# Optimization experiments

Hardware: AMD Instinct MI355X
Metric: run time of the kernel (lower is better)

## Reference

```python
import jax, jax.numpy as jnp
import numpy as np
from jax import lax

VOCAB, D, LAYERS, PAD = 10000, 200, 3, 3
B, S = 16, 512
SCALE = 0.05  # ~ torch uniform(-1/sqrt(200), 1/sqrt(200)) scale


def setup_inputs() -> dict:
    key = jax.random.key(0)
    ks = jax.random.split(key, 8)
    x = jax.random.randint(ks[0], (B, S), 0, VOCAB)
    emb = jax.random.normal(ks[1], (VOCAB, D), jnp.float32) * SCALE
    emb = emb.at[PAD].set(0.0)  # padding_idx=3 row is zeros
    w_ih = jax.random.normal(ks[2], (LAYERS, D, D), jnp.float32) * SCALE
    w_hh = jax.random.normal(ks[3], (LAYERS, D, D), jnp.float32) * SCALE
    b_ih = jax.random.normal(ks[4], (LAYERS, D), jnp.float32) * SCALE
    b_hh = jax.random.normal(ks[5], (LAYERS, D), jnp.float32) * SCALE
    fc_w = jax.random.normal(ks[6], (VOCAB, D), jnp.float32) * SCALE
    fc_b = jax.random.normal(ks[7], (VOCAB,), jnp.float32) * SCALE
    return {"x": x, "emb": emb, "w_ih": w_ih, "w_hh": w_hh,
            "b_ih": b_ih, "b_hh": b_hh, "fc_w": fc_w, "fc_b": fc_b}


def _rnn_forward(x, emb, w_ih, w_hh, b_ih, b_hh, fc_w, fc_b):
    h = emb[x]  # (B, S, D) embedding gather
    finals = []
    for l in range(LAYERS):
        # precompute input projection for the whole sequence (efficient GEMM)
        xw = jnp.einsum('bsd,hd->bsh', h, w_ih[l]) + b_ih[l] + b_hh[l]  # (B,S,D)
        w_hh_l_T = w_hh[l].T

        def step(h_prev, x_t):
            h_new = jnp.tanh(x_t + h_prev @ w_hh_l_T)
            return h_new, h_new

        h0 = jnp.zeros((x.shape[0], D), xw.dtype)
        h_last, outs = lax.scan(step, h0, jnp.swapaxes(xw, 0, 1))  # scan over time
        h = jnp.swapaxes(outs, 0, 1)  # (B, S, D)
        finals.append(h_last)
    hidden = jnp.stack(finals)  # (LAYERS, B, D) like torch RNN hidden
    logits = h @ fc_w.T + fc_b  # (B, S, VOCAB)
    return logits, hidden


def reference(x, emb, w_ih, w_hh, b_ih, b_hh, fc_w, fc_b):
    # forward always starts from zero hidden (source ignores the hidden arg)
    return _rnn_forward(x, emb, w_ih, w_hh, b_ih, b_hh, fc_w, fc_b)
```

## Files before the change

### kernel.cpp

```cpp
#include <hip/hip_runtime.h>
#include <hip/hip_bf16.h>

#define VOCAB 10000
#define D 200
#define NLAYERS 3
#define NB 16
#define NS 512
#define M 8192
#define KA 224
#define KB 232
#define NPADA 10120
#define NTILES_N 79
#define NT_TILES 5056
#define BCHUNKS 3712

#define OFF_BUF0 0u
#define OFF_BUF1 6553600u
#define OFF_WT   13107200u
#define OFF_HBF  13587200u
#define OFF_FWB  17257216u
#define OFF_STG1 21952896u
#define OFF_FLG  28506496u
#define WS_NEED  28506624u

typedef __bf16 bf16x8 __attribute__((ext_vector_type(8)));
typedef float  f32x4  __attribute__((ext_vector_type(4)));
typedef unsigned int u32x4 __attribute__((ext_vector_type(4)));
union U64x2 { unsigned long long d[2]; bf16x8 v; };

__global__ void k_wtrans(const float* __restrict__ w_ih, float* __restrict__ wt) {
    int i = blockIdx.x * blockDim.x + threadIdx.x;
    if (i < NLAYERS * D * D) {
        int l = i / (D * D);
        int r = i - l * D * D;
        int k = r / D;
        int n = r - k * D;
        wt[i] = w_ih[l * D * D + n * D + k];
    }
}

__global__ void k_fcwbf(const float* __restrict__ fc_w, __bf16* __restrict__ fwb) {
    int i = blockIdx.x * blockDim.x + threadIdx.x;
    if (i < NPADA * KB) {
        int n = i / KB;
        int k = i - n * KB;
        float v = (n < VOCAB && k < D) ? fc_w[(size_t)n * D + k] : 0.f;
        fwb[i] = (__bf16)v;
    }
}

__global__ void k_hbf2(const float* __restrict__ h, __bf16* __restrict__ hbf) {
    int i = blockIdx.x * blockDim.x + threadIdx.x;
    if (i < M * KA) {
        int m = i / KA;
        int k = i - m * KA;
        float v = (k < D) ? h[(size_t)m * D + k] : 0.f;
        hbf[i] = (__bf16)v;
    }
}

__global__ void k_zero(u32x4* __restrict__ p, int n4) {
    int i = blockIdx.x * blockDim.x + threadIdx.x;
    if (i < n4) p[i] = u32x4{0u, 0u, 0u, 0u};
}

__global__ void k_xw_emb(const int* __restrict__ x, const float* __restrict__ emb,
                         const float* __restrict__ wt,
                         const float* __restrict__ b_ih, const float* __restrict__ b_hh,
                         float* __restrict__ xw) {
    int m0 = blockIdx.x * 32;
    int n  = threadIdx.x;
    if (n >= D) return;
    float bias = b_ih[n] + b_hh[n];
    for (int g = 0; g < 8; ++g) {
        const float* r0 = emb + (size_t)x[m0 + g * 4 + 0] * D;
        const float* r1 = emb + (size_t)x[m0 + g * 4 + 1] * D;
        const float* r2 = emb + (size_t)x[m0 + g * 4 + 2] * D;
        const float* r3 = emb + (size_t)x[m0 + g * 4 + 3] * D;
        float a0 = bias, a1 = bias, a2 = bias, a3 = bias;
        for (int k = 0; k < D; k += 4) {
            #pragma unroll
            for (int kk = 0; kk < 4; ++kk) {
                float w = wt[(k + kk) * D + n];
                a0 += r0[k + kk] * w; a1 += r1[k + kk] * w;
                a2 += r2[k + kk] * w; a3 += r3[k + kk] * w;
            }
        }
        size_t o = (size_t)(m0 + g * 4) * D + n;
        xw[o] = a0; xw[o + D] = a1; xw[o + 2 * D] = a2; xw[o + 3 * D] = a3;
    }
}

__global__ void k_xw(const float* __restrict__ hin, const float* __restrict__ wt,
                     const float* __restrict__ b_ih, const float* __restrict__ b_hh,
                     float* __restrict__ xw) {
    int m0 = blockIdx.x * 32;
    int n  = threadIdx.x;
    if (n >= D) return;
    float bias = b_ih[n] + b_hh[n];
    for (int g = 0; g < 8; ++g) {
        const float* r0 = hin + (size_t)(m0 + g * 4) * D;
        float a0 = bias, a1 = bias, a2 = bias, a3 = bias;
        for (int k = 0; k < D; k += 4) {
            #pragma unroll
            for (int kk = 0; kk < 4; ++kk) {
                float w = wt[(k + kk) * D + n];
                a0 += r0[k + kk] * w; a1 += r0[D + k + kk] * w;
                a2 += r0[2 * D + k + kk] * w; a3 += r0[3 * D + k + kk] * w;
            }
        }
        size_t o = (size_t)(m0 + g * 4) * D + n;
        xw[o] = a0; xw[o + D] = a1; xw[o + 2 * D] = a2; xw[o + 3 * D] = a3;
    }
}

__device__ inline float fast_tanh(float x) {
    x = fminf(fmaxf(x, -15.f), 15.f);
    float e = __expf(2.f * x);
    return (e - 1.f) / (e + 1.f);
}

__global__ __attribute__((amdgpu_flat_work_group_size(512, 512),
                          amdgpu_waves_per_eu(2, 2)))
void k_fused(const float* __restrict__ whh_all,
             const float* __restrict__ wih_all,
             const float* __restrict__ b_ih,
             const float* __restrict__ b_hh,
             const float* __restrict__ xw0,
             unsigned* __restrict__ cells1,
             unsigned* __restrict__ cells2,
             __bf16* __restrict__ hbf,
             float* __restrict__ hidden,
             const __bf16* __restrict__ fwb,
             const float* __restrict__ fc_b,
             float* __restrict__ out,
             unsigned* __restrict__ progress,
             unsigned* __restrict__ counter) {
    __shared__ float hp0[208], hp1[208], hin[208];
    __shared__ __bf16 Bl[BCHUNKS * 8];
    __shared__ unsigned tile_s;
    const int bid = blockIdx.x;
    const int t   = threadIdx.x;

    if (bid < 48) {
        const int l   = bid >> 4;
        const int b   = bid & 15;
        const int q   = t >> 2, dg = t & 3;
        const bool act = (q < 100);
        const int  rr  = 2 * q + (dg & 1);
        const int  rrl = act ? rr : 0;
        const bool wlane = act && (dg < 2);
        const int  dstart = dg * 52;

        f32x4 wh[2][13], wi[2][13];
        #pragma unroll
        for (int j = 0; j < 2; ++j)
            #pragma unroll
            for (int i = 0; i < 13; ++i) {
                wh[j][i] = f32x4{0.f, 0.f, 0.f, 0.f};
                wi[j][i] = f32x4{0.f, 0.f, 0.f, 0.f};
            }
        if (act) {
            #pragma unroll
            for (int j = 0; j < 2; ++j) {
                const float* wr = whh_all + (size_t)l * D * D + (size_t)(2 * q + j) * D + dstart;
                #pragma unroll
                for (int i = 0; i < 11; ++i) wh[j][i] = *(const f32x4*)(wr + 4 * i);
                if (dg < 3) {
                    wh[j][11] = *(const f32x4*)(wr + 44);
                    wh[j][12] = *(const f32x4*)(wr + 48);
                }
            }
            if (l > 0) {
                #pragma unroll
                for (int j = 0; j < 2; ++j) {
                    const float* wr = wih_all + (size_t)l * D * D + (size_t)(2 * q + j) * D + dstart;
                    #pragma unroll
                    for (int i = 0; i < 11; ++i) wi[j][i] = *(const f32x4*)(wr + 4 * i);
                    if (dg < 3) {
                        wi[j][11] = *(const f32x4*)(wr + 44);
                        wi[j][12] = *(const f32x4*)(wr + 48);
                    }
                }
            }
        }
        float bias = 0.f;
        if (l > 0 && act) bias = b_ih[l * D + rr] + b_hh[l * D + rr];

        if (t < 208) { hp0[t] = 0.f; hp1[t] = 0.f; hin[t] = 0.f; }
        __syncthreads();

        const float* xrow = xw0 + (size_t)b * NS * D;
        const unsigned* sin = (l == 1) ? cells1 + (size_t)b * NS * 200
                            : (l == 2) ? cells2 + (size_t)b * NS * 200 : nullptr;
        unsigned* sout = (l == 0) ? cells1 + (size_t)b * NS * 200
                       : (l == 1) ? cells2 + (size_t)b * NS * 200 : nullptr;

        float hn_prev = 0.f;
        float xv_next = (l == 0) ? xrow[rrl] : 0.f;
        const float* hi = hin + dstart;

        #pragma unroll 1
        for (int s = 0; s < NS; ++s) {
            float xv;
            if (l == 0) {
                xv = xv_next;
                const int sn = (s + 1 < NS) ? s + 1 : NS - 1;
                xv_next = xrow[(size_t)sn * D + rrl];
            } else {
                if (t < 200) {
                    const unsigned* p = sin + (size_t)s * 200 + t;
                    unsigned v = __hip_atomic_load(p, __ATOMIC_RELAXED,
                                                   __HIP_MEMORY_SCOPE_AGENT);
                    while (v == 0u) {
                        __builtin_amdgcn_s_sleep(1);
                        v = __hip_atomic_load(p, __ATOMIC_RELAXED,
                                              __HIP_MEMORY_SCOPE_AGENT);
                    }
                    hin[t] = __builtin_bit_cast(float, ~v);
                }
                asm volatile("s_waitcnt lgkmcnt(0)" ::: "memory");
                __builtin_amdgcn_s_barrier();
                asm volatile("" ::: "memory");
                xv = bias;
            }
            const float* hr = ((s & 1) ? hp1 : hp0) + dstart;
            float* hw = (s & 1) ? hp0 : hp1;
            f32x4 ac0{0.f,0.f,0.f,0.f}, ac1{0.f,0.f,0.f,0.f};
            #pragma unroll
            for (int i = 0; i < 13; ++i) {
                f32x4 h4 = *(const f32x4*)(hr + 4 * i);
                ac0 += h4 * wh[0][i];
                ac1 += h4 * wh[1][i];
            }
            if (l > 0) {
                #pragma unroll
                for (int i = 0; i < 13; ++i) {
                    f32x4 g4 = *(const f32x4*)(hi + 4 * i);
                    ac0 += g4 * wi[0][i];
                    ac1 += g4 * wi[1][i];
                }
            }
            float s0 = (ac0.x + ac0.y) + (ac0.z + ac0.w);
            float s1 = (ac1.x + ac1.y) + (ac1.z + ac1.w);
            s0 += __shfl_xor(s0, 1);  s0 += __shfl_xor(s0, 2);
            s1 += __shfl_xor(s1, 1);  s1 += __shfl_xor(s1, 2);
            float hn = fast_tanh(xv + ((dg & 1) ? s1 : s0));
            hn_prev = hn;
            float hpart = __shfl_xor(hn, 1);
            if (wlane) {
                hw[rr] = hn;
                if (l < 2) {
                    __hip_atomic_store(sout + (size_t)s * 200 + rr,
                                       ~__builtin_bit_cast(unsigned, hn),
                                       __ATOMIC_RELAXED, __HIP_MEMORY_SCOPE_AGENT);
                }
            }
            if (l == 2 && act && dg == 0) {
                unsigned short e0 = __builtin_bit_cast(unsigned short, (__bf16)hn);
                unsigned short e1 = __builtin_bit_cast(unsigned short, (__bf16)hpart);
                unsigned pv = (unsigned)e0 | ((unsigned)e1 << 16);
                __hip_atomic_store((unsigned*)hbf + ((size_t)b * NS + s) * 112 + q,
                                   pv, __ATOMIC_RELAXED, __HIP_MEMORY_SCOPE_AGENT);
            }
            asm volatile("s_waitcnt lgkmcnt(0)" ::: "memory");
            __builtin_amdgcn_s_barrier();
            asm volatile("" ::: "memory");
            if (l == 2 && (s & 127) == 127) {
                asm volatile("s_waitcnt vmcnt(0)" ::: "memory");
                __builtin_amdgcn_s_barrier();
                if (t == 0)
                    __hip_atomic_store(progress + b, (unsigned)((s >> 7) + 1),
                                       __ATOMIC_RELAXED, __HIP_MEMORY_SCOPE_AGENT);
            }
        }
        if (wlane) hidden[(size_t)l * NB * D + b * D + rr] = hn_prev;
    } else {
        const int lane = t & 63, wv = t >> 6;
        const int wr = wv >> 2, wc = wv & 3;
        const int lr = lane & 15, lq = lane >> 4;
        const unsigned* Au = (const unsigned*)hbf;
        for (;;) {
            if (t == 0) tile_s = atomicAdd(counter, 1u);
            __syncthreads();
            const unsigned tile = tile_s;
            if (tile >= NT_TILES) break;
            const int chunk = tile / 1264;
            const int rem   = tile - chunk * 1264;
            const int nt    = rem >> 4;
            const int b     = rem & 15;
            const int m0    = (b * 4 + chunk) * 128;
            const int n0    = nt * 128;
            {
                const u32x4* src = (const u32x4*)(fwb + (size_t)n0 * KB);
                u32x4* dst = (u32x4*)Bl;
                #pragma unroll
                for (int it = 0; it < 8; ++it) {
                    int idx = t + it * 512;
                    if (idx < BCHUNKS) dst[idx] = src[idx];
                }
            }
            if (t == 0) {
                unsigned pv = __hip_atomic_load(progress + b, __ATOMIC_RELAXED,
                                                __HIP_MEMORY_SCOPE_AGENT);
                while (pv <= (unsigned)chunk) {
                    __builtin_amdgcn_s_sleep(16);
                    pv = __hip_atomic_load(progress + b, __ATOMIC_RELAXED,
                                           __HIP_MEMORY_SCOPE_AGENT);
                }
            }
            __syncthreads();
            f32x4 acc[4][2] = {};
            #pragma unroll
            for (int ks = 0; ks < 7; ++ks) {
                bf16x8 af[4], bfr[2];
                #pragma unroll
                for (int i = 0; i < 4; ++i) {
                    size_t arow = (size_t)(m0 + wr * 64 + i * 16 + lr);
                    size_t bo = arow * 112 + (size_t)(ks * 16 + lq * 4);
                    U64x2 u;
                    u.d[0] = __hip_atomic_load((const unsigned long long*)(Au + bo),
                                               __ATOMIC_RELAXED, __HIP_MEMORY_SCOPE_AGENT);
                    u.d[1] = __hip_atomic_load((const unsigned long long*)(Au + bo) + 1,
                                               __ATOMIC_RELAXED, __HIP_MEMORY_SCOPE_AGENT);
                    af[i] = u.v;
                }
                #pragma unroll
                for (int j = 0; j < 2; ++j) {
                    int brow = wc * 32 + j * 16 + lr;
                    bfr[j] = *(const bf16x8*)(Bl + brow * KB + (ks * 4 + lq) * 8);
                }
                #pragma unroll
                for (int i = 0; i < 4; ++i)
                    #pragma unroll
                    for (int j = 0; j < 2; ++j)
                        acc[i][j] = __builtin_amdgcn_mfma_f32_16x16x32_bf16(
                                        af[i], bfr[j], acc[i][j], 0, 0, 0);
            }
            #pragma unroll
            for (int j = 0; j < 2; ++j) {
                int col = n0 + wc * 32 + j * 16 + lr;
                if (col < VOCAB) {
                    float cbias = fc_b[col];
                    #pragma unroll
                    for (int i = 0; i < 4; ++i) {
                        #pragma unroll
                        for (int r = 0; r < 4; ++r) {
                            int row = m0 + wr * 64 + i * 16 + lq * 4 + r;
                            __builtin_nontemporal_store(acc[i][j][r] + cbias,
                                &out[(size_t)row * VOCAB + col]);
                        }
                    }
                }
            }
        }
    }
}

#define STEP(HR, HW, SIDX)                                                  \
    {                                                                       \
        float xv = xv_next;                                                 \
        int snext = (SIDX) + 1 < NS ? (SIDX) + 1 : NS - 1;                  \
        xv_next = xrow[(size_t)snext * D + rrl];                            \
        f32x4 ac0{0.f,0.f,0.f,0.f}, ac1{0.f,0.f,0.f,0.f};                   \
        _Pragma("unroll")                                                   \
        for (int i = 0; i < 13; ++i) {                                      \
            f32x4 h4 = *(const f32x4*)((HR) + 4 * i);                       \
            ac0 += h4 * w4[0][i];                                           \
            ac1 += h4 * w4[1][i];                                           \
        }                                                                   \
        float s0 = (ac0.x + ac0.y) + (ac0.z + ac0.w);                       \
        float s1 = (ac1.x + ac1.y) + (ac1.z + ac1.w);                       \
        s0 += __shfl_xor(s0, 1);  s0 += __shfl_xor(s0, 2);                  \
        s1 += __shfl_xor(s1, 1);  s1 += __shfl_xor(s1, 2);                  \
        float hn = fast_tanh(xv + ((dg & 1) ? s1 : s0));                    \
        hlast = hn;                                                         \
        if (wlane) {                                                        \
            (HW)[rr] = hn;                                                  \
            xrow[(size_t)(SIDX) * D + rr] = hn;                             \
        }                                                                   \
        __syncthreads();                                                    \
    }

__global__ __attribute__((amdgpu_flat_work_group_size(512, 512),
                          amdgpu_waves_per_eu(2, 2)))
void k_scan(const float* __restrict__ whh,
            float* __restrict__ io,
            float* __restrict__ hidden) {
    __shared__ float hp0[208], hp1[208];
    int t  = threadIdx.x;
    int b  = blockIdx.x;
    int q  = t >> 2;
    int dg = t & 3;
    const bool act = (q < 100);
    const int  rr  = 2 * q + (dg & 1);
    const int  rrl = act ? rr : 0;
    const bool wlane = act && (dg < 2);
    const int  dstart = dg * 52;

    f32x4 w4[2][13];
    #pragma unroll
    for (int j = 0; j < 2; ++j)
        #pragma unroll
        for (int i = 0; i < 13; ++i) w4[j][i] = f32x4{0.f, 0.f, 0.f, 0.f};
    if (act) {
        #pragma unroll
        for (int j = 0; j < 2; ++j) {
            const float* wr = whh + (size_t)(2 * q + j) * D + dstart;
            #pragma unroll
            for (int i = 0; i < 11; ++i) w4[j][i] = *(const f32x4*)(wr + 4 * i);
            if (dg < 3) {
                w4[j][11] = *(const f32x4*)(wr + 44);
                w4[j][12] = *(const f32x4*)(wr + 48);
            }
        }
    }
    if (t < 208) { hp0[t] = 0.f; hp1[t] = 0.f; }
    __syncthreads();

    float* xrow = io + (size_t)b * NS * D;
    const float* hr0 = hp0 + dstart;
    const float* hr1 = hp1 + dstart;
    float xv_next = xrow[rrl];
    float hlast = 0.f;

    #pragma unroll 1
    for (int s2 = 0; s2 < NS / 2; ++s2) {
        STEP(hr0, hp1, 2 * s2)
        STEP(hr1, hp0, 2 * s2 + 1)
    }
    if (wlane) hidden[b * D + rr] = hlast;
}

__global__ __launch_bounds__(256) void k_fc(const __bf16* __restrict__ A,
                                            const __bf16* __restrict__ Bw,
                                            const float* __restrict__ fc_b,
                                            float* __restrict__ Cout) {
    __shared__ __bf16 Bl2[3840 * 8];
    int tid = threadIdx.x;
    int wg  = blockIdx.x;
    int mt  = wg / NTILES_N, nt = wg - mt * NTILES_N;
    int m0  = mt * 128, n0 = nt * 128;
    {
        const u32x4* src = (const u32x4*)(Bw + (size_t)n0 * KB);
        u32x4* dst = (u32x4*)Bl2;
        u32x4 stg[15];
        #pragma unroll
        for (int it = 0; it < 15; ++it) stg[it] = src[tid + it * 256];
        #pragma unroll
        for (int it = 0; it < 15; ++it) dst[tid + it * 256] = stg[it];
    }
    __syncthreads();
    int lane = tid & 63, wv = tid >> 6;
    int wr = wv >> 1, wc = wv & 1;
    int lr = lane & 15, lq = lane >> 4;
    f32x4 acc[4][4] = {};
    #pragma unroll
    for (int ks = 0; ks < 7; ++ks) {
        bf16x8 af[4], bfr[4];
        #pragma unroll
        for (int i = 0; i < 4; ++i) {
            int arow = m0 + wr * 64 + i * 16 + lr;
            af[i] = *(const bf16x8*)(A + (size_t)arow * KA + (ks * 4 + lq) * 8);
            int brow = wc * 64 + i * 16 + lr;
            bfr[i] = *(const bf16x8*)(Bl2 + brow * KB + (ks * 4 + lq) * 8);
        }
        #pragma unroll
        for (int i = 0; i < 4; ++i)
            #pragma unroll
            for (int j = 0; j < 4; ++j)
                acc[i][j] = __builtin_amdgcn_mfma_f32_16x16x32_bf16(af[i], bfr[j],
                                                                   acc[i][j], 0, 0, 0);
    }
    #pragma unroll
    for (int j = 0; j < 4; ++j) {
        int col = n0 + wc * 64 + j * 16 + lr;
        if (col < VOCAB) {
            float bias = fc_b[col];
            #pragma unroll
            for (int i = 0; i < 4; ++i)
                #pragma unroll
                for (int r = 0; r < 4; ++r) {
                    int row = m0 + wr * 64 + i * 16 + lq * 4 + r;
                    __builtin_nontemporal_store(acc[i][j][r] + bias,
                                                &Cout[(size_t)row * VOCAB + col]);
                }
        }
    }
}

extern "C" void kernel_launch(void* const* d_in, const int* in_sizes, int n_in,
                              void* d_out, int out_size, void* d_ws, size_t ws_size,
                              hipStream_t stream) {
    const int*   x    = (const int*)  d_in[0];
    const float* emb  = (const float*)d_in[1];
    const float* w_ih = (const float*)d_in[2];
    const float* w_hh = (const float*)d_in[3];
    const float* b_ih = (const float*)d_in[4];
    const float* b_hh = (const float*)d_in[5];
    const float* fc_w = (const float*)d_in[6];
    const float* fc_b = (const float*)d_in[7];
    float* out    = (float*)d_out;
    float* hidden = out + (size_t)M * VOCAB;

    char* ws = (char*)d_ws;
    float*    buf0 = (float*)(ws + OFF_BUF0);
    float*    buf1 = (float*)(ws + OFF_BUF1);
    float*    wt   = (float*)(ws + OFF_WT);
    __bf16*   hbf  = (__bf16*)(ws + OFF_HBF);
    __bf16*   fwb  = (__bf16*)(ws + OFF_FWB);
    unsigned* stg0 = (unsigned*)(ws + OFF_BUF0);
    unsigned* stg1 = (unsigned*)(ws + OFF_STG1);
    unsigned* flg  = (unsigned*)(ws + OFF_FLG);

    k_wtrans<<<(NLAYERS * D * D + 255) / 256, 256, 0, stream>>>(w_ih, wt);
    k_fcwbf <<<(NPADA * KB + 255) / 256, 256, 0, stream>>>(fc_w, fwb);

    if (ws_size >= WS_NEED) {
        k_xw_emb<<<M / 32, 256, 0, stream>>>(x, emb, wt, b_ih, b_hh, buf1);
        const int nst4 = NB * NS * 200 / 4;
        const int nhb4 = M * KA * 2 / 16;
        k_zero<<<(nst4 + 255) / 256, 256, 0, stream>>>((u32x4*)stg0, nst4);
        k_zero<<<(nst4 + 255) / 256, 256, 0, stream>>>((u32x4*)stg1, nst4);
        k_zero<<<(nhb4 + 255) / 256, 256, 0, stream>>>((u32x4*)hbf, nhb4);
        k_zero<<<1, 256, 0, stream>>>((u32x4*)flg, 8);
        k_fused<<<256, 512, 0, stream>>>(w_hh, w_ih, b_ih, b_hh, buf1,
                                         stg0, stg1, hbf, hidden,
                                         fwb, fc_b, out, flg, flg + 16);
    } else {
        k_xw_emb<<<M / 32, 256, 0, stream>>>(x, emb, wt, b_ih, b_hh, buf1);
        k_scan<<<NB, 512, 0, stream>>>(w_hh, buf1, hidden);
        float* cur = buf1;
        float* nxt = buf0;
        for (int l = 1; l < NLAYERS; ++l) {
            k_xw  <<<M / 32, 256, 0, stream>>>(cur, wt + l * D * D,
                                               b_ih + l * D, b_hh + l * D, nxt);
            k_scan<<<NB, 512, 0, stream>>>(w_hh + (size_t)l * D * D, nxt,
                                           hidden + l * NB * D);
            float* tswap = cur; cur = nxt; nxt = tswap;
        }
        k_hbf2<<<(M * KA + 255) / 256, 256, 0, stream>>>(cur, hbf);
        k_fc<<<64 * NTILES_N, 256, 0, stream>>>(hbf, fwb, fc_b, out);
    }
}
```

Baseline: 839.8 us.

## Fold layer-0 input projection into fused scan and merge prep kernels

Layer-0 blocks now gather embedding rows per step and apply the input-projection weights in registers, the same way layers 1 and 2 already do. This removes the separate k_xw_emb GEMM launch and the xw buffer round trip. The bf16 conversion of fc_w and the zeroing of staging and flag buffers are merged into one grid-stride prep kernel. The full hbf zeroing is dropped because layer-2 threads now write the padding columns inline. In exchange, every layer-0 step carries extra FMA work and a dependent embedding load on the serial recurrence path.

Result: faster. 730.1 us, median of 2 (-13.1%).

```diff
diff --git a/kernel.cpp b/kernel.cpp
--- a/kernel.cpp
+++ b/kernel.cpp
@@ -28,6 +28,25 @@
 typedef unsigned int u32x4 __attribute__((ext_vector_type(4)));
 union U64x2 { unsigned long long d[2]; bf16x8 v; };
 
+__global__ void k_prep(const float* __restrict__ fc_w, __bf16* __restrict__ fwb,
+                       u32x4* __restrict__ c1, u32x4* __restrict__ c2,
+                       unsigned* __restrict__ flg) {
+    const int i = blockIdx.x * blockDim.x + threadIdx.x;
+    const int stride = gridDim.x * blockDim.x;
+    for (int j = i; j < NPADA * KB; j += stride) {
+        int n = j / KB;
+        int k = j - n * KB;
+        float v = (n < VOCAB && k < D) ? fc_w[(size_t)n * D + k] : 0.f;
+        fwb[j] = (__bf16)v;
+    }
+    const int nst4 = NB * NS * 200 / 4;
+    for (int j = i; j < nst4; j += stride) {
+        c1[j] = u32x4{0u, 0u, 0u, 0u};
+        c2[j] = u32x4{0u, 0u, 0u, 0u};
+    }
+    if (i < 32) flg[i] = 0u;
+}
+
 __global__ void k_wtrans(const float* __restrict__ w_ih, float* __restrict__ wt) {
     int i = blockIdx.x * blockDim.x + threadIdx.x;
     if (i < NLAYERS * D * D) {
@@ -57,11 +76,6 @@
         float v = (k < D) ? h[(size_t)m * D + k] : 0.f;
         hbf[i] = (__bf16)v;
     }
-}
-
-__global__ void k_zero(u32x4* __restrict__ p, int n4) {
-    int i = blockIdx.x * blockDim.x + threadIdx.x;
-    if (i < n4) p[i] = u32x4{0u, 0u, 0u, 0u};
 }
 
 __global__ void k_xw_emb(const int* __restrict__ x, const float* __restrict__ emb,
@@ -126,7 +140,8 @@
              const float* __restrict__ wih_all,
              const float* __restrict__ b_ih,
              const float* __restrict__ b_hh,
-             const float* __restrict__ xw0,
+             const int* __restrict__ x,
+             const float* __restrict__ emb,
              unsigned* __restrict__ cells1,
              unsigned* __restrict__ cells2,
              __bf16* __restrict__ hbf,
@@ -137,6 +152,7 @@
              unsigned* __restrict__ progress,
              unsigned* __restrict__ counter) {
     __shared__ float hp0[208], hp1[208], hin[208];
+    __shared__ int xtok[NS];
     __shared__ __bf16 Bl[BCHUNKS * 8];
     __shared__ unsigned tile_s;
     const int bid = blockIdx.x;
@@ -148,7 +164,6 @@
         const int q   = t >> 2, dg = t & 3;
         const bool act = (q < 100);
         const int  rr  = 2 * q + (dg & 1);
-        const int  rrl = act ? rr : 0;
         const bool wlane = act && (dg < 2);
         const int  dstart = dg * 52;
 
@@ -171,44 +186,41 @@
                     wh[j][12] = *(const f32x4*)(wr + 48);
                 }
             }
-            if (l > 0) {
-                #pragma unroll
-                for (int j = 0; j < 2; ++j) {
-                    const float* wr = wih_all + (size_t)l * D * D + (size_t)(2 * q + j) * D + dstart;
-                    #pragma unroll
-                    for (int i = 0; i < 11; ++i) wi[j][i] = *(const f32x4*)(wr + 4 * i);
-                    if (dg < 3) {
-                        wi[j][11] = *(const f32x4*)(wr + 44);
-                        wi[j][12] = *(const f32x4*)(wr + 48);
-                    }
+            #pragma unroll
+            for (int j = 0; j < 2; ++j) {
+                const float* wr = wih_all + (size_t)l * D * D + (size_t)(2 * q + j) * D + dstart;
+                #pragma unroll
+                for (int i = 0; i < 11; ++i) wi[j][i] = *(const f32x4*)(wr + 4 * i);
+                if (dg < 3) {
+                    wi[j][11] = *(const f32x4*)(wr + 44);
+                    wi[j][12] = *(const f32x4*)(wr + 48);
                 }
             }
         }
         float bias = 0.f;
-        if (l > 0 && act) bias = b_ih[l * D + rr] + b_hh[l * D + rr];
+        if (act) bias = b_ih[l * D + rr] + b_hh[l * D + rr];
 
         if (t < 208) { hp0[t] = 0.f; hp1[t] = 0.f; hin[t] = 0.f; }
+        if (l == 0)
+            for (int i = t; i < NS; i += 512) xtok[i] = x[b * NS + i];
         __syncthreads();
 
-        const float* xrow = xw0 + (size_t)b * NS * D;
         const unsigned* sin = (l == 1) ? cells1 + (size_t)b * NS * 200
                             : (l == 2) ? cells2 + (size_t)b * NS * 200 : nullptr;
         unsigned* sout = (l == 0) ? cells1 + (size_t)b * NS * 200
                        : (l == 1) ? cells2 + (size_t)b * NS * 200 : nullptr;
 
         float hn_prev = 0.f;
-        float xv_next = (l == 0) ? xrow[rrl] : 0.f;
+        float ereg = 0.f;
+        if (l == 0 && t < 200) ereg = emb[(size_t)xtok[0] * D + t];
         const float* hi = hin + dstart;
 
         #pragma unroll 1
         for (int s = 0; s < NS; ++s) {
-            float xv;
-            if (l == 0) {
-                xv = xv_next;
-                const int sn = (s + 1 < NS) ? s + 1 : NS - 1;
-                xv_next = xrow[(size_t)sn * D + rrl];
-            } else {
-                if (t < 200) {
+            if (t < 200) {
+                if (l == 0) {
+                    hin[t] = ereg;
+                } else {
                     const unsigned* p = sin + (size_t)s * 200 + t;
                     unsigned v = __hip_atomic_load(p, __ATOMIC_RELAXED,
                                                    __HIP_MEMORY_SCOPE_AGENT);
@@ -219,10 +231,13 @@
                     }
                     hin[t] = __builtin_bit_cast(float, ~v);
                 }
-                asm volatile("s_waitcnt lgkmcnt(0)" ::: "memory");
-                __builtin_amdgcn_s_barrier();
-                asm volatile("" ::: "memory");
-                xv = bias;
+            }
+            asm volatile("s_waitcnt lgkmcnt(0)" ::: "memory");
+            __builtin_amdgcn_s_barrier();
+            asm volatile("" ::: "memory");
+            if (l == 0 && t < 200) {
+                const int sn = (s + 1 < NS) ? s + 1 : NS - 1;
+                ereg = emb[(size_t)xtok[sn] * D + t];
             }
             const float* hr = ((s & 1) ? hp1 : hp0) + dstart;
             float* hw = (s & 1) ? hp0 : hp1;
@@ -233,19 +248,17 @@
                 ac0 += h4 * wh[0][i];
                 ac1 += h4 * wh[1][i];
             }
-            if (l > 0) {
-                #pragma unroll
-                for (int i = 0; i < 13; ++i) {
-                    f32x4 g4 = *(const f32x4*)(hi + 4 * i);
-                    ac0 += g4 * wi[0][i];
-                    ac1 += g4 * wi[1][i];
-                }
+            #pragma unroll
+            for (int i = 0; i < 13; ++i) {
+                f32x4 g4 = *(const f32x4*)(hi + 4 * i);
+                ac0 += g4 * wi[0][i];
+                ac1 += g4 * wi[1][i];
             }
             float s0 = (ac0.x + ac0.y) + (ac0.z + ac0.w);
             float s1 = (ac1.x + ac1.y) + (ac1.z + ac1.w);
             s0 += __shfl_xor(s0, 1);  s0 += __shfl_xor(s0, 2);
             s1 += __shfl_xor(s1, 1);  s1 += __shfl_xor(s1, 2);
-            float hn = fast_tanh(xv + ((dg & 1) ? s1 : s0));
+            float hn = fast_tanh(bias + ((dg & 1) ? s1 : s0));
             hn_prev = hn;
             float hpart = __shfl_xor(hn, 1);
             if (wlane) {
@@ -256,12 +269,18 @@
                                        __ATOMIC_RELAXED, __HIP_MEMORY_SCOPE_AGENT);
                 }
             }
-            if (l == 2 && act && dg == 0) {
-                unsigned short e0 = __builtin_bit_cast(unsigned short, (__bf16)hn);
-                unsigned short e1 = __builtin_bit_cast(unsigned short, (__bf16)hpart);
-                unsigned pv = (unsigned)e0 | ((unsigned)e1 << 16);
-                __hip_atomic_store((unsigned*)hbf + ((size_t)b * NS + s) * 112 + q,
-                                   pv, __ATOMIC_RELAXED, __HIP_MEMORY_SCOPE_AGENT);
+            if (l == 2) {
+                if (act && dg == 0) {
+                    unsigned short e0 = __builtin_bit_cast(unsigned short, (__bf16)hn);
+                    unsigned short e1 = __builtin_bit_cast(unsigned short, (__bf16)hpart);
+                    unsigned pv = (unsigned)e0 | ((unsigned)e1 << 16);
+                    __hip_atomic_store((unsigned*)hbf + ((size_t)b * NS + s) * 112 + q,
+                                       pv, __ATOMIC_RELAXED, __HIP_MEMORY_SCOPE_AGENT);
+                } else if (t >= 400 && t < 412) {
+                    __hip_atomic_store((unsigned*)hbf + ((size_t)b * NS + s) * 112
+                                           + 100 + (t - 400),
+                                       0u, __ATOMIC_RELAXED, __HIP_MEMORY_SCOPE_AGENT);
+                }
             }
             asm volatile("s_waitcnt lgkmcnt(0)" ::: "memory");
             __builtin_amdgcn_s_barrier();
@@ -513,21 +532,14 @@
     unsigned* stg1 = (unsigned*)(ws + OFF_STG1);
     unsigned* flg  = (unsigned*)(ws + OFF_FLG);
 
-    k_wtrans<<<(NLAYERS * D * D + 255) / 256, 256, 0, stream>>>(w_ih, wt);
-    k_fcwbf <<<(NPADA * KB + 255) / 256, 256, 0, stream>>>(fc_w, fwb);
-
     if (ws_size >= WS_NEED) {
-        k_xw_emb<<<M / 32, 256, 0, stream>>>(x, emb, wt, b_ih, b_hh, buf1);
-        const int nst4 = NB * NS * 200 / 4;
-        const int nhb4 = M * KA * 2 / 16;
-        k_zero<<<(nst4 + 255) / 256, 256, 0, stream>>>((u32x4*)stg0, nst4);
-        k_zero<<<(nst4 + 255) / 256, 256, 0, stream>>>((u32x4*)stg1, nst4);
-        k_zero<<<(nhb4 + 255) / 256, 256, 0, stream>>>((u32x4*)hbf, nhb4);
-        k_zero<<<1, 256, 0, stream>>>((u32x4*)flg, 8);
-        k_fused<<<256, 512, 0, stream>>>(w_hh, w_ih, b_ih, b_hh, buf1,
+        k_prep<<<2048, 256, 0, stream>>>(fc_w, fwb, (u32x4*)stg0, (u32x4*)stg1, flg);
+        k_fused<<<256, 512, 0, stream>>>(w_hh, w_ih, b_ih, b_hh, x, emb,
                                          stg0, stg1, hbf, hidden,
                                          fwb, fc_b, out, flg, flg + 16);
     } else {
+        k_wtrans<<<(NLAYERS * D * D + 255) / 256, 256, 0, stream>>>(w_ih, wt);
+        k_fcwbf <<<(NPADA * KB + 255) / 256, 256, 0, stream>>>(fc_w, fwb);
         k_xw_emb<<<M / 32, 256, 0, stream>>>(x, emb, wt, b_ih, b_hh, buf1);
         k_scan<<<NB, 512, 0, stream>>>(w_hh, buf1, hidden);
         float* cur = buf1;
```
